# Performance work log

Hardware: AMD Instinct MI355X
Metric: run time of the kernel (lower is better)

The kernel has to match this reference:

```python
import jax, jax.numpy as jnp
import numpy as np

D_MODEL = 1024
NUM_HEADS = 16
HEAD_DIM = D_MODEL // NUM_HEADS
HIDDEN = 4096
EPS = 1e-10


def _layernorm(x, gamma, beta):
    mean = jnp.mean(x, axis=-1, keepdims=True)
    var = jnp.var(x, axis=-1, keepdims=True)  # unbiased=False
    return gamma * (x - mean) / jnp.sqrt(var + EPS) + beta


def setup_inputs() -> dict:
    key = jax.random.key(0)
    ks = jax.random.split(key, 16)
    s = 0.02
    d, h = D_MODEL, HIDDEN
    inp = {
        "x": jax.random.normal(ks[0], (4, 2048, d), dtype=jnp.float32),
        "Wq": jax.random.normal(ks[1], (d, d), dtype=jnp.float32) * s,
        "bq": jnp.zeros((d,), jnp.float32),
        "Wk": jax.random.normal(ks[2], (d, d), dtype=jnp.float32) * s,
        "bk": jnp.zeros((d,), jnp.float32),
        "Wv": jax.random.normal(ks[3], (d, d), dtype=jnp.float32) * s,
        "bv": jnp.zeros((d,), jnp.float32),
        "Wo": jax.random.normal(ks[4], (d, d), dtype=jnp.float32) * s,
        "bo": jnp.zeros((d,), jnp.float32),
        "W1": jax.random.normal(ks[5], (d, h), dtype=jnp.float32) * s,
        "b1": jnp.zeros((h,), jnp.float32),
        "W2": jax.random.normal(ks[6], (h, d), dtype=jnp.float32) * s,
        "b2": jnp.zeros((d,), jnp.float32),
        "gamma1": jnp.ones((d,), jnp.float32),
        "beta1": jnp.zeros((d,), jnp.float32),
        "gamma2": jnp.ones((d,), jnp.float32),
        "beta2": jnp.zeros((d,), jnp.float32),
    }
    return inp


def reference(x, Wq, bq, Wk, bk, Wv, bv, Wo, bo, W1, b1, W2, b2,
              gamma1, beta1, gamma2, beta2):
    B, S, D = x.shape
    H, hd = NUM_HEADS, HEAD_DIM
    scale = jnp.sqrt(jnp.float32(hd))

    # --- sublayer 1: self-attention on norm(x), residual add ---
    xn = _layernorm(x, gamma1, beta1)
    Q = (xn @ Wq + bq).reshape(B, S, H, hd).transpose(0, 2, 1, 3)  # [B,H,S,hd]
    K = (xn @ Wk + bk).reshape(B, S, H, hd).transpose(0, 2, 1, 3)
    V = (xn @ Wv + bv).reshape(B, S, H, hd).transpose(0, 2, 1, 3)
    scores = jnp.einsum("bhqd,bhkd->bhqk", Q, K) / scale  # [B,H,S,S]
    attn = jax.nn.softmax(scores, axis=-1)
    ctx = jnp.einsum("bhqk,bhkd->bhqd", attn, V)  # [B,H,S,hd]
    ctx = ctx.transpose(0, 2, 1, 3).reshape(B, S, D)
    x = x + (ctx @ Wo + bo)

    # --- sublayer 2: FFN on norm(x), residual add ---
    xn = _layernorm(x, gamma2, beta2)
    h = jax.nn.gelu(xn @ W1 + b1, approximate=False)  # torch F.gelu default = erf
    x = x + (h @ W2 + b2)
    return x
```

## Files before the change

kernel.cpp:

```cpp
#include <hip/hip_runtime.h>
#include <stdint.h>

#define D_MODEL 1024
#define HIDDEN  4096
#define SEQ     2048
#define NTOK    8192
#define NHEAD   16
#define HDIM    64

typedef unsigned short u16;
typedef __attribute__((ext_vector_type(8))) __bf16 bf16x8;
typedef __attribute__((ext_vector_type(4))) float f32x4;

__device__ __forceinline__ u16 f2bf(float f) {
  union { float f; unsigned u; } c; c.f = f;
  unsigned u = c.u + 0x7fffu + ((c.u >> 16) & 1u);
  return (u16)(u >> 16);
}

__device__ __forceinline__ void gload16(const void* g, void* l) {
  __builtin_amdgcn_global_load_lds((const __attribute__((address_space(1))) void*)g,
                                   (__attribute__((address_space(3))) void*)l, 16, 0, 0);
}

__global__ void transpose_cvt(const float* __restrict__ W, u16* __restrict__ Wt, int K, int N) {
  __shared__ float t[32][33];
  const int k0 = blockIdx.y * 32, n0 = blockIdx.x * 32;
  const int tx = threadIdx.x, ty = threadIdx.y;
#pragma unroll
  for (int p = 0; p < 4; ++p)
    t[ty + p * 8][tx] = W[(size_t)(k0 + ty + p * 8) * N + n0 + tx];
  __syncthreads();
#pragma unroll
  for (int p = 0; p < 4; ++p) {
    const int n = ty + p * 8;
    Wt[(size_t)(n0 + n) * K + k0 + tx] = f2bf(t[tx][n]);
  }
}

__global__ __launch_bounds__(256)
void ln_kernel(const float* __restrict__ x, const float* __restrict__ gamma,
               const float* __restrict__ beta, u16* __restrict__ out) {
  const int row = blockIdx.x;
  const int tid = threadIdx.x;
  const float4 v = ((const float4*)(x + (size_t)row * D_MODEL))[tid];
  float s = v.x + v.y + v.z + v.w;
  float q = v.x * v.x + v.y * v.y + v.z * v.z + v.w * v.w;
#pragma unroll
  for (int o = 32; o > 0; o >>= 1) { s += __shfl_down(s, o); q += __shfl_down(q, o); }
  __shared__ float ps[4], pq[4];
  const int wid = tid >> 6, lane = tid & 63;
  if (lane == 0) { ps[wid] = s; pq[wid] = q; }
  __syncthreads();
  s = ps[0] + ps[1] + ps[2] + ps[3];
  q = pq[0] + pq[1] + pq[2] + pq[3];
  const float mean = s * (1.0f / D_MODEL);
  const float var = q * (1.0f / D_MODEL) - mean * mean;
  const float rstd = rsqrtf(var + 1e-10f);
  const float4 gv = ((const float4*)gamma)[tid];
  const float4 bv = ((const float4*)beta)[tid];
  ushort4 o4;
  o4.x = f2bf((v.x - mean) * rstd * gv.x + bv.x);
  o4.y = f2bf((v.y - mean) * rstd * gv.y + bv.y);
  o4.z = f2bf((v.z - mean) * rstd * gv.z + bv.z);
  o4.w = f2bf((v.w - mean) * rstd * gv.w + bv.w);
  ((ushort4*)(out + (size_t)row * D_MODEL))[tid] = o4;
}

#define SLOT_AE (256 * 32)
#define SLOT_BE (128 * 32)
#define SLOT_E  (SLOT_AE + SLOT_BE)
#define SLOT_BYTES (SLOT_E * 2)

template <int EPI, int KPY, int KPX>
__global__ __launch_bounds__(512, 4)
void gemm32(const u16* __restrict__ A, const u16* __restrict__ Bt,
            const float* __restrict__ bias, const float* __restrict__ bias2,
            const float* __restrict__ res, void* __restrict__ outp, void* __restrict__ outp2,
            int M, int N, int K) {
  __shared__ u16 Ls[3 * SLOT_E];
  const int tid = threadIdx.x;
  const int wid = tid >> 6, lane = tid & 63;
  const int g = lane >> 4, lr = lane & 15;
  const int wr = wid >> 1, wc = wid & 1;

  const int xcd = blockIdx.x & 7, l = blockIdx.x >> 3;
  int bx, by;
  if (KPY > 0) { by = xcd * KPY + (l % KPY); bx = l / KPY; }
  else         { bx = xcd * KPX + (l % KPX); by = l / KPX; }
  const int m0 = by * 256, n0 = bx * 128;

  const int NT = K >> 5;

  const int rA0 = tid >> 2, cc0 = ((tid & 3) ^ (rA0 & 3)) << 3;
  const int u1 = tid + 512;
  const int rA1 = u1 >> 2, cc1 = (((u1 & 3) ^ (rA1 & 3))) << 3;
  const u16* pA0 = A + (size_t)(m0 + rA0) * K + cc0;
  const u16* pA1 = A + (size_t)(m0 + rA1) * K + cc1;
  const u16* pB0 = Bt + (size_t)(n0 + rA0) * K + cc0;
  const int dA0 = wid * 1024;
  const int dA1 = wid * 1024 + 8192;
  const int dB0 = SLOT_AE * 2 + wid * 1024;

  auto stage = [&](int slot) {
    char* sb = (char*)Ls + slot * SLOT_BYTES;
    gload16(pA0, sb + dA0);
    gload16(pA1, sb + dA1);
    gload16(pB0, sb + dB0);
    pA0 += 32; pA1 += 32; pB0 += 32;
  };

  stage(0); stage(1); stage(2);

  f32x4 acc[4][4] = {};
  const int cx = (g ^ (lr & 3)) << 3;

  for (int t = 0; t < NT; ++t) {
    if (t + 3 <= NT)      asm volatile("s_waitcnt vmcnt(6)" ::: "memory");
    else if (t + 2 <= NT) asm volatile("s_waitcnt vmcnt(3)" ::: "memory");
    else                  asm volatile("s_waitcnt vmcnt(0)" ::: "memory");
    asm volatile("s_barrier" ::: "memory");

    const int slot = t % 3;
    const u16* sA = Ls + slot * SLOT_E;
    const u16* sB = sA + SLOT_AE;
    bf16x8 af[4], bfr[4];
#pragma unroll
    for (int mf = 0; mf < 4; ++mf)
      af[mf] = *(const bf16x8*)(sA + (wr * 64 + mf * 16 + lr) * 32 + cx);
#pragma unroll
    for (int nf = 0; nf < 4; ++nf)
      bfr[nf] = *(const bf16x8*)(sB + (wc * 64 + nf * 16 + lr) * 32 + cx);

    __builtin_amdgcn_s_setprio(1);
#pragma unroll
    for (int mf = 0; mf < 4; ++mf)
#pragma unroll
      for (int nf = 0; nf < 4; ++nf)
        acc[mf][nf] = __builtin_amdgcn_mfma_f32_16x16x32_bf16(af[mf], bfr[nf], acc[mf][nf], 0, 0, 0);
    __builtin_amdgcn_s_setprio(0);

    if (t + 3 < NT) {
      asm volatile("s_barrier" ::: "memory");
      stage(slot);
    }
  }

#pragma unroll
  for (int mf = 0; mf < 4; ++mf)
#pragma unroll
    for (int nf = 0; nf < 4; ++nf) {
      const int gn = n0 + wc * 64 + nf * 16 + lr;
      const int gm = m0 + wr * 64 + mf * 16 + 4 * g;
#pragma unroll
      for (int r = 0; r < 4; ++r) {
        const float av = acc[mf][nf][r];
        if (EPI == 0) {
          ((u16*)outp)[(size_t)(gm + r) * N + gn] = f2bf(av + bias[gn]);
        } else if (EPI == 1) {
          const size_t idx = (size_t)(gm + r) * N + gn;
          ((float*)outp)[idx] = av + bias[gn] + res[idx];
        } else if (EPI == 2) {
          const float v = av + bias[gn];
          ((u16*)outp)[(size_t)(gm + r) * N + gn] =
              f2bf(0.5f * v * (1.0f + erff(v * 0.7071067811865475f)));
        } else if (EPI == 3) {
          const int gn_p = (gn & ~63) | ((gn & 15) << 2) | ((gn >> 4) & 3);
          ((u16*)outp)[(size_t)(gm + r) * N + gn_p] = f2bf(av + bias[gm + r]);
        } else {
          const int side = gn >> 10, col = gn & 1023;
          u16* o = (u16*)(side ? outp2 : outp);
          float t_ = av + (side ? bias2[col] : bias[col]);
          if (!side) t_ *= 0.125f;
          o[(size_t)(gm + r) * 1024 + col] = f2bf(t_);
        }
      }
    }
}

__global__ __launch_bounds__(256, 2)
void attn_kernel(const u16* __restrict__ Q, const u16* __restrict__ K,
                 const u16* __restrict__ Vt, u16* __restrict__ ctxo) {
  const int bh = blockIdx.y;
  const int b = bh >> 4, h = bh & 15;
  const int q0 = blockIdx.x * 256;
  const int tid = threadIdx.x, wid = tid >> 6, lane = tid & 63;
  const int g = lane >> 4, lr = lane & 15;
  const size_t base = ((size_t)b * SEQ) * D_MODEL + h * HDIM;
  const size_t vbase = ((size_t)h * HDIM) * NTOK + (size_t)b * SEQ;

  __shared__ u16 Ks[64 * 72];
  __shared__ u16 Vts[64 * 72];
  __shared__ u16 Ps[128 * 72];

  const int qw = wid * 32;

  bf16x8 aq[2][2][2];
#pragma unroll
  for (int qt = 0; qt < 2; ++qt) {
    __syncthreads();
#pragma unroll
    for (int i = 0; i < 4; ++i) {
      const int ch = tid + 256 * i, row = ch >> 3, j = ch & 7;
      *(bf16x8*)(Ps + row * 72 + j * 8) =
          *(const bf16x8*)(Q + base + (size_t)(q0 + qt * 128 + row) * D_MODEL + j * 8);
    }
    __syncthreads();
#pragma unroll
    for (int qf = 0; qf < 2; ++qf)
#pragma unroll
      for (int ks = 0; ks < 2; ++ks)
        aq[qt][qf][ks] = *(const bf16x8*)(Ps + (qw + qf * 16 + lr) * 72 + ks * 32 + g * 8);
  }

  f32x4 o[2][2][4] = {};
  float lrun[2][2][4] = {};

  for (int kv0 = 0; kv0 < SEQ; kv0 += 64) {
    __syncthreads();
#pragma unroll
    for (int i = 0; i < 2; ++i) {
      const int row = (tid >> 3) + i * 32, j = tid & 7;
      *(bf16x8*)(Ks + row * 72 + j * 8) =
          *(const bf16x8*)(K + base + (size_t)(kv0 + row) * D_MODEL + j * 8);
      *(bf16x8*)(Vts + row * 72 + j * 8) =
          *(const bf16x8*)(Vt + vbase + (size_t)row * NTOK + kv0 + j * 8);
    }
    __syncthreads();

#pragma unroll
    for (int qt = 0; qt < 2; ++qt) {
      f32x4 s[2][4] = {};
      __builtin_amdgcn_s_setprio(1);
#pragma unroll
      for (int ks = 0; ks < 2; ++ks)
#pragma unroll
        for (int kf = 0; kf < 4; ++kf) {
          const bf16x8 bk = *(const bf16x8*)(Ks + (kf * 16 + lr) * 72 + ks * 32 + g * 8);
#pragma unroll
          for (int qf = 0; qf < 2; ++qf)
            s[qf][kf] =
                __builtin_amdgcn_mfma_f32_16x16x32_bf16(aq[qt][qf][ks], bk, s[qf][kf], 0, 0, 0);
        }
      __builtin_amdgcn_s_setprio(0);

#pragma unroll
      for (int qf = 0; qf < 2; ++qf)
#pragma unroll
        for (int r = 0; r < 4; ++r) {
          union { float f; unsigned u; } p0, p1, p2, p3;
          p0.f = __expf(s[qf][0][r]);
          p1.f = __expf(s[qf][1][r]);
          p2.f = __expf(s[qf][2][r]);
          p3.f = __expf(s[qf][3][r]);
          lrun[qt][qf][r] += (p0.f + p1.f) + (p2.f + p3.f);
          const unsigned lo = __builtin_amdgcn_perm(p1.u + 0x8000u, p0.u + 0x8000u, 0x07060302u);
          const unsigned hi = __builtin_amdgcn_perm(p3.u + 0x8000u, p2.u + 0x8000u, 0x07060302u);
          *(uint2*)(Ps + (qw + qf * 16 + 4 * g + r) * 72 + lr * 4) = make_uint2(lo, hi);
        }
      asm volatile("s_waitcnt lgkmcnt(0)" ::: "memory");

      __builtin_amdgcn_s_setprio(1);
#pragma unroll
      for (int ks = 0; ks < 2; ++ks) {
        bf16x8 pf[2];
#pragma unroll
        for (int qf = 0; qf < 2; ++qf)
          pf[qf] = *(const bf16x8*)(Ps + (qw + qf * 16 + lr) * 72 + ks * 32 + g * 8);
#pragma unroll
        for (int df = 0; df < 4; ++df) {
          const bf16x8 vf = *(const bf16x8*)(Vts + (df * 16 + lr) * 72 + ks * 32 + g * 8);
#pragma unroll
          for (int qf = 0; qf < 2; ++qf)
            o[qt][qf][df] =
                __builtin_amdgcn_mfma_f32_16x16x32_bf16(pf[qf], vf, o[qt][qf][df], 0, 0, 0);
        }
      }
      __builtin_amdgcn_s_setprio(0);
    }
  }

#pragma unroll
  for (int off = 1; off < 16; off <<= 1)
#pragma unroll
    for (int qt = 0; qt < 2; ++qt)
#pragma unroll
      for (int qf = 0; qf < 2; ++qf)
#pragma unroll
        for (int r = 0; r < 4; ++r)
          lrun[qt][qf][r] += __shfl_xor(lrun[qt][qf][r], off);

#pragma unroll
  for (int qt = 0; qt < 2; ++qt)
#pragma unroll
    for (int qf = 0; qf < 2; ++qf)
#pragma unroll
      for (int r = 0; r < 4; ++r) {
        const float rinv = 1.0f / lrun[qt][qf][r];
        const int qrow = q0 + qt * 128 + qw + qf * 16 + 4 * g + r;
#pragma unroll
        for (int df = 0; df < 4; ++df)
          ctxo[base + (size_t)qrow * D_MODEL + df * 16 + lr] = f2bf(o[qt][qf][df][r] * rinv);
      }
}

extern "C" void kernel_launch(void* const* d_in, const int* in_sizes, int n_in,
                              void* d_out, int out_size, void* d_ws, size_t ws_size,
                              hipStream_t stream) {
  const float* x  = (const float*)d_in[0];
  const float* Wq = (const float*)d_in[1];
  const float* bq = (const float*)d_in[2];
  const float* Wk = (const float*)d_in[3];
  const float* bk = (const float*)d_in[4];
  const float* Wv = (const float*)d_in[5];
  const float* bv = (const float*)d_in[6];
  const float* Wo = (const float*)d_in[7];
  const float* bo = (const float*)d_in[8];
  const float* W1 = (const float*)d_in[9];
  const float* b1 = (const float*)d_in[10];
  const float* W2 = (const float*)d_in[11];
  const float* b2 = (const float*)d_in[12];
  const float* gamma1 = (const float*)d_in[13];
  const float* beta1  = (const float*)d_in[14];
  const float* gamma2 = (const float*)d_in[15];
  const float* beta2  = (const float*)d_in[16];
  float* out = (float*)d_out;

  const size_t M1 = 1u << 20;
  u16* w   = (u16*)d_ws;
  u16* WtQ = w;
  u16* WtK = w + 1 * M1;
  u16* WtV = w + 2 * M1;
  u16* WtO = w + 3 * M1;
  u16* Wt1 = w + 4 * M1;
  u16* Wt2 = w + 8 * M1;
  u16* xn  = w + 12 * M1;
  u16* Qb  = w + 20 * M1;
  u16* Kb  = w + 28 * M1;
  u16* Vtb = w + 36 * M1;
  u16* ctx = w + 44 * M1;
  u16* hb  = w + 20 * M1;
  float* x1 = (float*)(w + 52 * M1);

  const dim3 tb(32, 8);
  transpose_cvt<<<dim3(D_MODEL / 32, D_MODEL / 32), tb, 0, stream>>>(Wq, WtQ, D_MODEL, D_MODEL);
  transpose_cvt<<<dim3(D_MODEL / 32, D_MODEL / 32), tb, 0, stream>>>(Wk, WtK, D_MODEL, D_MODEL);
  transpose_cvt<<<dim3(D_MODEL / 32, D_MODEL / 32), tb, 0, stream>>>(Wv, WtV, D_MODEL, D_MODEL);
  transpose_cvt<<<dim3(D_MODEL / 32, D_MODEL / 32), tb, 0, stream>>>(Wo, WtO, D_MODEL, D_MODEL);
  transpose_cvt<<<dim3(HIDDEN / 32, D_MODEL / 32), tb, 0, stream>>>(W1, Wt1, D_MODEL, HIDDEN);
  transpose_cvt<<<dim3(D_MODEL / 32, HIDDEN / 32), tb, 0, stream>>>(W2, Wt2, HIDDEN, D_MODEL);

  ln_kernel<<<NTOK, 256, 0, stream>>>(x, gamma1, beta1, xn);

  gemm32<6, 4, 0><<<512, 512, 0, stream>>>(xn, WtQ, bq, bk, nullptr, Qb, Kb,
                                           NTOK, 2048, D_MODEL);
  gemm32<3, 0, 8><<<256, 512, 0, stream>>>(WtV, xn, bv, nullptr, nullptr, Vtb, nullptr,
                                           D_MODEL, NTOK, D_MODEL);

  attn_kernel<<<dim3(SEQ / 256, 64), 256, 0, stream>>>(Qb, Kb, Vtb, ctx);

  gemm32<1, 4, 0><<<256, 512, 0, stream>>>(ctx, WtO, bo, nullptr, x, x1, nullptr,
                                           NTOK, D_MODEL, D_MODEL);

  ln_kernel<<<NTOK, 256, 0, stream>>>(x1, gamma2, beta2, xn);

  gemm32<2, 4, 0><<<1024, 512, 0, stream>>>(xn, Wt1, b1, nullptr, nullptr, hb, nullptr,
                                            NTOK, HIDDEN, D_MODEL);
  gemm32<1, 4, 0><<<256, 512, 0, stream>>>(hb, Wt2, b2, nullptr, x1, out, nullptr,
                                           NTOK, D_MODEL, HIDDEN);
}
```

Measured before the change: 407.4 us.

## Shrink attention tiles to 128 queries, remap grid, and batch weight transposes

The attention kernel now handles 128 query rows per block instead of 256, launching 1024 blocks in a 1D grid. A swizzled mapping groups eight heads together for K/V cache locality, and the launch bound is raised to 4 blocks per CU for higher occupancy. It also pads the LDS stride from 72 to 76 to reduce bank conflicts, switches to the native v_exp_f32 with log2e folded into the Q scale, and uses the hardware packed bf16 convert. The four square weight transposes are merged into one launch. The trade-off is that K/V tiles are reloaded twice as often per query row, and the bf16 rounding changes slightly.

```diff
diff --git a/kernel.cpp b/kernel.cpp
--- a/kernel.cpp
+++ b/kernel.cpp
@@ -21,6 +21,26 @@
 __device__ __forceinline__ void gload16(const void* g, void* l) {
   __builtin_amdgcn_global_load_lds((const __attribute__((address_space(1))) void*)g,
                                    (__attribute__((address_space(3))) void*)l, 16, 0, 0);
+}
+
+__global__ void transpose_cvt4(const float* __restrict__ A0, const float* __restrict__ A1,
+                               const float* __restrict__ A2, const float* __restrict__ A3,
+                               u16* __restrict__ O) {
+  __shared__ float t[32][33];
+  const int z = blockIdx.z;
+  const float* W = (z == 0) ? A0 : (z == 1) ? A1 : (z == 2) ? A2 : A3;
+  u16* Wt = O + ((size_t)z << 20);
+  const int k0 = blockIdx.y * 32, n0 = blockIdx.x * 32;
+  const int tx = threadIdx.x, ty = threadIdx.y;
+#pragma unroll
+  for (int p = 0; p < 4; ++p)
+    t[ty + p * 8][tx] = W[(size_t)(k0 + ty + p * 8) * D_MODEL + n0 + tx];
+  __syncthreads();
+#pragma unroll
+  for (int p = 0; p < 4; ++p) {
+    const int n = ty + p * 8;
+    Wt[(size_t)(n0 + n) * D_MODEL + k0 + tx] = f2bf(t[tx][n]);
+  }
 }
 
 __global__ void transpose_cvt(const float* __restrict__ W, u16* __restrict__ Wt, int K, int N) {
@@ -171,137 +191,128 @@
           const int side = gn >> 10, col = gn & 1023;
           u16* o = (u16*)(side ? outp2 : outp);
           float t_ = av + (side ? bias2[col] : bias[col]);
-          if (!side) t_ *= 0.125f;
+          if (!side) t_ *= 0.18033688011112042f;
           o[(size_t)(gm + r) * 1024 + col] = f2bf(t_);
         }
       }
     }
 }
 
-__global__ __launch_bounds__(256, 2)
+__global__ __launch_bounds__(256, 4)
 void attn_kernel(const u16* __restrict__ Q, const u16* __restrict__ K,
                  const u16* __restrict__ Vt, u16* __restrict__ ctxo) {
-  const int bh = blockIdx.y;
+  const int L = blockIdx.x;
+  const int q0 = ((L >> 3) & 15) * 128;
+  const int bh = ((L >> 7) << 3) | (L & 7);
   const int b = bh >> 4, h = bh & 15;
-  const int q0 = blockIdx.x * 256;
   const int tid = threadIdx.x, wid = tid >> 6, lane = tid & 63;
   const int g = lane >> 4, lr = lane & 15;
   const size_t base = ((size_t)b * SEQ) * D_MODEL + h * HDIM;
   const size_t vbase = ((size_t)h * HDIM) * NTOK + (size_t)b * SEQ;
 
-  __shared__ u16 Ks[64 * 72];
-  __shared__ u16 Vts[64 * 72];
-  __shared__ u16 Ps[128 * 72];
+#define AST 76
+  __shared__ u16 Ks[64 * AST];
+  __shared__ u16 Vts[64 * AST];
+  __shared__ u16 Ps[128 * AST];
 
   const int qw = wid * 32;
 
-  bf16x8 aq[2][2][2];
-#pragma unroll
-  for (int qt = 0; qt < 2; ++qt) {
-    __syncthreads();
-#pragma unroll
-    for (int i = 0; i < 4; ++i) {
-      const int ch = tid + 256 * i, row = ch >> 3, j = ch & 7;
-      *(bf16x8*)(Ps + row * 72 + j * 8) =
-          *(const bf16x8*)(Q + base + (size_t)(q0 + qt * 128 + row) * D_MODEL + j * 8);
-    }
-    __syncthreads();
-#pragma unroll
-    for (int qf = 0; qf < 2; ++qf)
-#pragma unroll
-      for (int ks = 0; ks < 2; ++ks)
-        aq[qt][qf][ks] = *(const bf16x8*)(Ps + (qw + qf * 16 + lr) * 72 + ks * 32 + g * 8);
-  }
-
-  f32x4 o[2][2][4] = {};
-  float lrun[2][2][4] = {};
+#pragma unroll
+  for (int i = 0; i < 4; ++i) {
+    const int ch = tid + 256 * i, row = ch >> 3, j = ch & 7;
+    *(bf16x8*)(Ps + row * AST + j * 8) =
+        *(const bf16x8*)(Q + base + (size_t)(q0 + row) * D_MODEL + j * 8);
+  }
+  __syncthreads();
+  bf16x8 aq[2][2];
+#pragma unroll
+  for (int qf = 0; qf < 2; ++qf)
+#pragma unroll
+    for (int ks = 0; ks < 2; ++ks)
+      aq[qf][ks] = *(const bf16x8*)(Ps + (qw + qf * 16 + lr) * AST + ks * 32 + g * 8);
+
+  f32x4 o[2][4] = {};
+  float lrun[2][4] = {};
 
   for (int kv0 = 0; kv0 < SEQ; kv0 += 64) {
     __syncthreads();
 #pragma unroll
     for (int i = 0; i < 2; ++i) {
       const int row = (tid >> 3) + i * 32, j = tid & 7;
-      *(bf16x8*)(Ks + row * 72 + j * 8) =
+      *(bf16x8*)(Ks + row * AST + j * 8) =
           *(const bf16x8*)(K + base + (size_t)(kv0 + row) * D_MODEL + j * 8);
-      *(bf16x8*)(Vts + row * 72 + j * 8) =
+      *(bf16x8*)(Vts + row * AST + j * 8) =
           *(const bf16x8*)(Vt + vbase + (size_t)row * NTOK + kv0 + j * 8);
     }
     __syncthreads();
 
-#pragma unroll
-    for (int qt = 0; qt < 2; ++qt) {
-      f32x4 s[2][4] = {};
-      __builtin_amdgcn_s_setprio(1);
-#pragma unroll
-      for (int ks = 0; ks < 2; ++ks)
-#pragma unroll
-        for (int kf = 0; kf < 4; ++kf) {
-          const bf16x8 bk = *(const bf16x8*)(Ks + (kf * 16 + lr) * 72 + ks * 32 + g * 8);
-#pragma unroll
-          for (int qf = 0; qf < 2; ++qf)
-            s[qf][kf] =
-                __builtin_amdgcn_mfma_f32_16x16x32_bf16(aq[qt][qf][ks], bk, s[qf][kf], 0, 0, 0);
-        }
-      __builtin_amdgcn_s_setprio(0);
-
+    f32x4 s[2][4] = {};
+    __builtin_amdgcn_s_setprio(1);
+#pragma unroll
+    for (int ks = 0; ks < 2; ++ks)
+#pragma unroll
+      for (int kf = 0; kf < 4; ++kf) {
+        const bf16x8 bk = *(const bf16x8*)(Ks + (kf * 16 + lr) * AST + ks * 32 + g * 8);
+#pragma unroll
+        for (int qf = 0; qf < 2; ++qf)
+          s[qf][kf] = __builtin_amdgcn_mfma_f32_16x16x32_bf16(aq[qf][ks], bk, s[qf][kf], 0, 0, 0);
+      }
+    __builtin_amdgcn_s_setprio(0);
+
+#pragma unroll
+    for (int qf = 0; qf < 2; ++qf)
+#pragma unroll
+      for (int r = 0; r < 4; ++r) {
+        float p0, p1, p2, p3;
+        asm("v_exp_f32 %0, %1" : "=v"(p0) : "v"(s[qf][0][r]));
+        asm("v_exp_f32 %0, %1" : "=v"(p1) : "v"(s[qf][1][r]));
+        asm("v_exp_f32 %0, %1" : "=v"(p2) : "v"(s[qf][2][r]));
+        asm("v_exp_f32 %0, %1" : "=v"(p3) : "v"(s[qf][3][r]));
+        lrun[qf][r] += (p0 + p1) + (p2 + p3);
+        unsigned lo, hi;
+        asm("v_cvt_pk_bf16_f32 %0, %1, %2" : "=v"(lo) : "v"(p0), "v"(p1));
+        asm("v_cvt_pk_bf16_f32 %0, %1, %2" : "=v"(hi) : "v"(p2), "v"(p3));
+        *(uint2*)(Ps + (qw + qf * 16 + 4 * g + r) * AST + lr * 4) = make_uint2(lo, hi);
+      }
+    asm volatile("s_waitcnt lgkmcnt(0)" ::: "memory");
+
+    __builtin_amdgcn_s_setprio(1);
+#pragma unroll
+    for (int ks = 0; ks < 2; ++ks) {
+      bf16x8 pf[2];
 #pragma unroll
       for (int qf = 0; qf < 2; ++qf)
-#pragma unroll
-        for (int r = 0; r < 4; ++r) {
-          union { float f; unsigned u; } p0, p1, p2, p3;
-          p0.f = __expf(s[qf][0][r]);
-          p1.f = __expf(s[qf][1][r]);
-          p2.f = __expf(s[qf][2][r]);
-          p3.f = __expf(s[qf][3][r]);
-          lrun[qt][qf][r] += (p0.f + p1.f) + (p2.f + p3.f);
-          const unsigned lo = __builtin_amdgcn_perm(p1.u + 0x8000u, p0.u + 0x8000u, 0x07060302u);
-          const unsigned hi = __builtin_amdgcn_perm(p3.u + 0x8000u, p2.u + 0x8000u, 0x07060302u);
-          *(uint2*)(Ps + (qw + qf * 16 + 4 * g + r) * 72 + lr * 4) = make_uint2(lo, hi);
-        }
-      asm volatile("s_waitcnt lgkmcnt(0)" ::: "memory");
-
-      __builtin_amdgcn_s_setprio(1);
-#pragma unroll
-      for (int ks = 0; ks < 2; ++ks) {
-        bf16x8 pf[2];
+        pf[qf] = *(const bf16x8*)(Ps + (qw + qf * 16 + lr) * AST + ks * 32 + g * 8);
+#pragma unroll
+      for (int df = 0; df < 4; ++df) {
+        const bf16x8 vf = *(const bf16x8*)(Vts + (df * 16 + lr) * AST + ks * 32 + g * 8);
 #pragma unroll
         for (int qf = 0; qf < 2; ++qf)
-          pf[qf] = *(const bf16x8*)(Ps + (qw + qf * 16 + lr) * 72 + ks * 32 + g * 8);
-#pragma unroll
-        for (int df = 0; df < 4; ++df) {
-          const bf16x8 vf = *(const bf16x8*)(Vts + (df * 16 + lr) * 72 + ks * 32 + g * 8);
-#pragma unroll
-          for (int qf = 0; qf < 2; ++qf)
-            o[qt][qf][df] =
-                __builtin_amdgcn_mfma_f32_16x16x32_bf16(pf[qf], vf, o[qt][qf][df], 0, 0, 0);
-        }
+          o[qf][df] = __builtin_amdgcn_mfma_f32_16x16x32_bf16(pf[qf], vf, o[qf][df], 0, 0, 0);
       }
-      __builtin_amdgcn_s_setprio(0);
-    }
+    }
+    __builtin_amdgcn_s_setprio(0);
   }
 
 #pragma unroll
   for (int off = 1; off < 16; off <<= 1)
 #pragma unroll
-    for (int qt = 0; qt < 2; ++qt)
-#pragma unroll
-      for (int qf = 0; qf < 2; ++qf)
-#pragma unroll
-        for (int r = 0; r < 4; ++r)
-          lrun[qt][qf][r] += __shfl_xor(lrun[qt][qf][r], off);
-
-#pragma unroll
-  for (int qt = 0; qt < 2; ++qt)
-#pragma unroll
     for (int qf = 0; qf < 2; ++qf)
 #pragma unroll
-      for (int r = 0; r < 4; ++r) {
-        const float rinv = 1.0f / lrun[qt][qf][r];
-        const int qrow = q0 + qt * 128 + qw + qf * 16 + 4 * g + r;
-#pragma unroll
-        for (int df = 0; df < 4; ++df)
-          ctxo[base + (size_t)qrow * D_MODEL + df * 16 + lr] = f2bf(o[qt][qf][df][r] * rinv);
-      }
+      for (int r = 0; r < 4; ++r)
+        lrun[qf][r] += __shfl_xor(lrun[qf][r], off);
+
+#pragma unroll
+  for (int qf = 0; qf < 2; ++qf)
+#pragma unroll
+    for (int r = 0; r < 4; ++r) {
+      const float rinv = 1.0f / lrun[qf][r];
+      const int qrow = q0 + qw + qf * 16 + 4 * g + r;
+#pragma unroll
+      for (int df = 0; df < 4; ++df)
+        ctxo[base + (size_t)qrow * D_MODEL + df * 16 + lr] = f2bf(o[qf][df][r] * rinv);
+    }
+#undef AST
 }
 
 extern "C" void kernel_launch(void* const* d_in, const int* in_sizes, int n_in,
@@ -329,7 +340,6 @@
   const size_t M1 = 1u << 20;
   u16* w   = (u16*)d_ws;
   u16* WtQ = w;
-  u16* WtK = w + 1 * M1;
   u16* WtV = w + 2 * M1;
   u16* WtO = w + 3 * M1;
   u16* Wt1 = w + 4 * M1;
@@ -343,10 +353,7 @@
   float* x1 = (float*)(w + 52 * M1);
 
   const dim3 tb(32, 8);
-  transpose_cvt<<<dim3(D_MODEL / 32, D_MODEL / 32), tb, 0, stream>>>(Wq, WtQ, D_MODEL, D_MODEL);
-  transpose_cvt<<<dim3(D_MODEL / 32, D_MODEL / 32), tb, 0, stream>>>(Wk, WtK, D_MODEL, D_MODEL);
-  transpose_cvt<<<dim3(D_MODEL / 32, D_MODEL / 32), tb, 0, stream>>>(Wv, WtV, D_MODEL, D_MODEL);
-  transpose_cvt<<<dim3(D_MODEL / 32, D_MODEL / 32), tb, 0, stream>>>(Wo, WtO, D_MODEL, D_MODEL);
+  transpose_cvt4<<<dim3(32, 32, 4), tb, 0, stream>>>(Wq, Wk, Wv, Wo, WtQ);
   transpose_cvt<<<dim3(HIDDEN / 32, D_MODEL / 32), tb, 0, stream>>>(W1, Wt1, D_MODEL, HIDDEN);
   transpose_cvt<<<dim3(D_MODEL / 32, HIDDEN / 32), tb, 0, stream>>>(W2, Wt2, HIDDEN, D_MODEL);
 
@@ -357,7 +364,7 @@
   gemm32<3, 0, 8><<<256, 512, 0, stream>>>(WtV, xn, bv, nullptr, nullptr, Vtb, nullptr,
                                            D_MODEL, NTOK, D_MODEL);
 
-  attn_kernel<<<dim3(SEQ / 256, 64), 256, 0, stream>>>(Qb, Kb, Vtb, ctx);
+  attn_kernel<<<1024, 256, 0, stream>>>(Qb, Kb, Vtb, ctx);
 
   gemm32<1, 4, 0><<<256, 512, 0, stream>>>(ctx, WtO, bo, nullptr, x, x1, nullptr,
                                            NTOK, D_MODEL, D_MODEL);
```

Result: faster. 384.6 us (-5.6%).
